# Kernel optimization log

Measured on AMD Instinct MI355X. Metric: run time of the kernel, lower is better.

Reference implementation:

```python
import jax, jax.numpy as jnp
import numpy as np

N = 2048       # nodes (also onehot length)
E = 32768      # edges (avg degree 16)
C_IN = 128
C_OUT = 128
OH_CH = 8
BN_EPS = 1e-5


def _conv1d(x, w):
    # x: [N, Cin, L], w: [Cout, Cin, 3], padding 1 (SAME)
    return jax.lax.conv_general_dilated(
        x, w, window_strides=(1,), padding=[(1, 1)],
        dimension_numbers=('NCH', 'OIH', 'NCH'))


def setup_inputs() -> dict:
    key = jax.random.key(0)
    ks = jax.random.split(key, 16)
    x = jax.random.normal(ks[0], (N, C_IN), dtype=jnp.float32)
    onehot = jax.random.uniform(ks[1], (N, N), dtype=jnp.float32)
    adj = jax.random.randint(ks[2], (2, E), 0, N)

    def lin(k, fan_in, shape):
        return jax.random.normal(k, shape, dtype=jnp.float32) / np.sqrt(fan_in)

    # first_linear: (C_IN + OH_CH) -> C_OUT  (stored as [in, out])
    W1 = lin(ks[3], C_IN + OH_CH, (C_IN + OH_CH, C_OUT))
    b1 = jnp.zeros((C_OUT,), jnp.float32)
    # mlp: BatchNorm1d(C_OUT) -> ReLU -> Linear(C_OUT, C_OUT)
    gamma = jnp.ones((C_OUT,), jnp.float32)
    beta = jnp.zeros((C_OUT,), jnp.float32)
    W2 = lin(ks[4], C_OUT, (C_OUT, C_OUT))
    b2 = jnp.zeros((C_OUT,), jnp.float32)
    # onehot_pipe: Conv1d(1,8,3) -> ReLU -> Conv1d(8,16,3) -> ReLU -> avgpool -> Linear(16, OH_CH)
    cw1 = lin(ks[5], 1 * 3, (8, 1, 3)); cb1 = jnp.zeros((8,), jnp.float32)
    cw2 = lin(ks[6], 8 * 3, (16, 8, 3)); cb2 = jnp.zeros((16,), jnp.float32)
    Wr = lin(ks[7], 16, (16, OH_CH)); br = jnp.zeros((OH_CH,), jnp.float32)

    return {"x": x, "onehot": onehot, "adj": adj, "n_nodes": N,
            "W1": W1, "b1": b1, "gamma": gamma, "beta": beta,
            "W2": W2, "b2": b2, "cw1": cw1, "cb1": cb1,
            "cw2": cw2, "cb2": cb2, "Wr": Wr, "br": br}


def reference(x, onehot, adj, n_nodes, W1, b1, gamma, beta, W2, b2,
              cw1, cb1, cw2, cb2, Wr, br):
    send, recv = adj[0], adj[1]
    # propagate: gather at senders, scatter-add at receivers
    agg_x = jax.ops.segment_sum(x[send], recv, num_segments=n_nodes)          # [N, C_IN]
    agg_oh = jax.ops.segment_sum(onehot[send], recv, num_segments=n_nodes)    # [N, N]
    new_oh = onehot + agg_oh                                                  # update()

    # onehot_pipe on sorted onehot rows
    s = jnp.sort(new_oh, axis=-1)[:, None, :]                                 # [N, 1, L]
    h = jax.nn.relu(_conv1d(s, cw1) + cb1[None, :, None])                     # [N, 8, L]
    h = jax.nn.relu(_conv1d(h, cw2) + cb2[None, :, None])                     # [N, 16, L]
    h = h.mean(axis=-1)                                                       # AdaptiveAvgPool1d(1)+Flatten
    readout = h @ Wr + br                                                     # [N, OH_CH]

    x2 = jnp.concatenate([agg_x, readout], axis=1)                            # hstack
    x2 = x2 @ W1 + b1                                                         # first_linear
    # BatchNorm1d in training mode (batch stats, biased variance)
    mu = x2.mean(axis=0)
    var = x2.var(axis=0)
    x2 = (x2 - mu) * jax.lax.rsqrt(var + BN_EPS) * gamma + beta
    x2 = jax.nn.relu(x2)
    x2 = x2 @ W2 + b2
    return (x2, new_oh)
```

## Files before the change

### kernel.cpp

```cpp
#include <hip/hip_runtime.h>
#include <hip/hip_bf16.h>
#include <math.h>

#define NN   2048
#define LROW 2048
#define DEGCAP 128

typedef __attribute__((ext_vector_type(8))) short short8;
typedef __attribute__((ext_vector_type(4))) float f32x4;
typedef unsigned int u32;

__device__ __forceinline__ unsigned short bf16b(float x) {
    __hip_bfloat16 h = __float2bfloat16(x);
    return *reinterpret_cast<unsigned short*>(&h);
}


__device__ __forceinline__ u32 pkmin(u32 a, u32 b) {
    u32 d; asm("v_pk_min_f16 %0, %1, %2" : "=v"(d) : "v"(a), "v"(b)); return d;
}
__device__ __forceinline__ u32 pkmax(u32 a, u32 b) {
    u32 d; asm("v_pk_max_f16 %0, %1, %2" : "=v"(d) : "v"(a), "v"(b)); return d;
}
__device__ __forceinline__ u32 packf2(float lo, float hi) {
    union { _Float16 h[2]; u32 u; } c;
    c.h[0] = (_Float16)lo; c.h[1] = (_Float16)hi;
    return c.u;
}
__device__ __forceinline__ float unpk_lo(u32 v) {
    union { u32 u; _Float16 h[2]; } c; c.u = v; return (float)c.h[0];
}
__device__ __forceinline__ float unpk_hi(u32 v) {
    union { u32 u; _Float16 h[2]; } c; c.u = v; return (float)c.h[1];
}


__global__ __launch_bounds__(256) void prep_k(
        const float* __restrict__ oh, unsigned short* __restrict__ ohbf,
        const int* __restrict__ send, const int* __restrict__ recv,
        int* __restrict__ cnt, int* __restrict__ elist2, int E) {
    const int bid = blockIdx.x;
    if (bid < NN) {
        int base = bid * 2048 + threadIdx.x * 8;
        float4 f0 = *(const float4*)(oh + base);
        float4 f1 = *(const float4*)(oh + base + 4);
        union { short8 s8; unsigned short us[8]; } pk;
        pk.us[0] = bf16b(f0.x); pk.us[1] = bf16b(f0.y);
        pk.us[2] = bf16b(f0.z); pk.us[3] = bf16b(f0.w);
        pk.us[4] = bf16b(f1.x); pk.us[5] = bf16b(f1.y);
        pk.us[6] = bf16b(f1.z); pk.us[7] = bf16b(f1.w);
        *(short8*)(ohbf + base) = pk.s8;
    } else {
        int i = (bid - NN) * 256 + threadIdx.x;
        if (i < E) {
            int r = recv[i];
            int slot = atomicAdd(&cnt[r], 1);
            if (slot < DEGCAP) elist2[r * DEGCAP + slot] = send[i];
        }
    }
}

__global__ void fill2_k(const int* __restrict__ send, const int* __restrict__ recv,
                        int* __restrict__ cnt, int* __restrict__ elist2, int E) {
    int i = blockIdx.x * blockDim.x + threadIdx.x;
    if (i >= E) return;
    int r = recv[i];
    int slot = atomicAdd(&cnt[r], 1);
    if (slot < DEGCAP) elist2[r * DEGCAP + slot] = send[i];
}


__device__ __forceinline__ void ce(float& a, float& b, bool up) {
    float lo = fminf(a, b), hi = fmaxf(a, b);
    a = up ? lo : hi;
    b = up ? hi : lo;
}

__device__ __forceinline__ void ce_pk(u32& a, u32& b, bool up) {
    u32 mn = pkmin(a, b), mx = pkmax(a, b);
    a = up ? mn : mx;
    b = up ? mx : mn;
}

__device__ __forceinline__ void merge8_pk(u32 h[4], bool up) {
    ce_pk(h[0], h[2], up); ce_pk(h[1], h[3], up);
    ce_pk(h[0], h[1], up); ce_pk(h[2], h[3], up);
#pragma unroll
    for (int m = 0; m < 4; ++m) {
        u32 hs = (h[m] >> 16) | (h[m] << 16);
        u32 mn = pkmin(h[m], hs);
        u32 mx = pkmax(h[m], hs);
        u32 ru = __builtin_amdgcn_perm(mx, mn, 0x07060100u);
        u32 rd = __builtin_amdgcn_perm(mn, mx, 0x07060100u);
        h[m] = up ? ru : rd;
    }
}

__device__ __forceinline__ short8 conv1pack(float xm, float x0v, float xp,
        const float* __restrict__ cw1, const float* __restrict__ cb1) {
    union { short8 s8; unsigned short us[8]; } pk;
#pragma unroll
    for (int c = 0; c < 8; ++c) {
        float w = cb1[c] + cw1[c * 3] * xm + cw1[c * 3 + 1] * x0v + cw1[c * 3 + 2] * xp;
        pk.us[c] = bf16b(w > 0.f ? w : 0.f);
    }
    return pk.s8;
}


template<int BF>
__global__ __launch_bounds__(256, 8) void fused_k(
        const float* __restrict__ oh, const unsigned short* __restrict__ ohbf,
        const float* __restrict__ x,
        const int* __restrict__ elist2, const int* __restrict__ cnt,
        float* __restrict__ newoh, float* __restrict__ t,
        const float* __restrict__ cw1, const float* __restrict__ cb1,
        const float* __restrict__ cw2, const float* __restrict__ cb2,
        const float* __restrict__ Wr,  const float* __restrict__ br,
        const float* __restrict__ W1,  const float* __restrict__ b1) {
    __shared__ __align__(16) char smem[1028 * 16];
    float* sf = (float*)smem;
    u32* sfu = (u32*)smem;
    unsigned short* h1t = (unsigned short*)smem;
    __shared__ unsigned short a_lds[16 * 32];
    __shared__ float red[4][16];
    __shared__ float u[136];
    __shared__ float lpart[128];

    const int r = blockIdx.x, tid = threadIdx.x;
    const int lane = tid & 63, wv = tid >> 6;
    const int col = tid * 8;

    for (int i = tid; i < 512; i += 256) {
        int c2 = i >> 5, k = i & 31, d = k >> 3, c1 = k & 7;
        float w = (d < 3) ? cw2[(c2 * 8 + c1) * 3 + d] : 0.f;
        a_lds[i] = bf16b(w);
    }

    float v[8];
    {
        float4 b0 = *(const float4*)(oh + (size_t)r * LROW + col);
        float4 b1v = *(const float4*)(oh + (size_t)r * LROW + col + 4);
        v[0] = b0.x;  v[1] = b0.y;  v[2] = b0.z;  v[3] = b0.w;
        v[4] = b1v.x; v[5] = b1v.y; v[6] = b1v.z; v[7] = b1v.w;
    }
    float myagg = 0.f;
    const int deg = min(cnt[r], DEGCAP);
    const int* my = elist2 + r * DEGCAP;
    int e = 0;
    if (BF) {
        for (; e + 4 <= deg; e += 4) {
            int se0 = my[e], se1 = my[e + 1], se2 = my[e + 2], se3 = my[e + 3];
            uint4 ua = *((const uint4*)(ohbf + (size_t)se0 * LROW) + tid);
            uint4 ub = *((const uint4*)(ohbf + (size_t)se1 * LROW) + tid);
            uint4 uc = *((const uint4*)(ohbf + (size_t)se2 * LROW) + tid);
            uint4 ud = *((const uint4*)(ohbf + (size_t)se3 * LROW) + tid);
            float xa = 0.f, xb = 0.f, xc = 0.f, xd = 0.f;
            if (tid < 128) {
                xa = x[(size_t)se0 * 128 + tid]; xb = x[(size_t)se1 * 128 + tid];
                xc = x[(size_t)se2 * 128 + tid]; xd = x[(size_t)se3 * 128 + tid];
            }
            v[0] += __uint_as_float(ua.x << 16); v[1] += __uint_as_float(ua.x & 0xffff0000u);
            v[2] += __uint_as_float(ua.y << 16); v[3] += __uint_as_float(ua.y & 0xffff0000u);
            v[4] += __uint_as_float(ua.z << 16); v[5] += __uint_as_float(ua.z & 0xffff0000u);
            v[6] += __uint_as_float(ua.w << 16); v[7] += __uint_as_float(ua.w & 0xffff0000u);
            v[0] += __uint_as_float(ub.x << 16); v[1] += __uint_as_float(ub.x & 0xffff0000u);
            v[2] += __uint_as_float(ub.y << 16); v[3] += __uint_as_float(ub.y & 0xffff0000u);
            v[4] += __uint_as_float(ub.z << 16); v[5] += __uint_as_float(ub.z & 0xffff0000u);
            v[6] += __uint_as_float(ub.w << 16); v[7] += __uint_as_float(ub.w & 0xffff0000u);
            v[0] += __uint_as_float(uc.x << 16); v[1] += __uint_as_float(uc.x & 0xffff0000u);
            v[2] += __uint_as_float(uc.y << 16); v[3] += __uint_as_float(uc.y & 0xffff0000u);
            v[4] += __uint_as_float(uc.z << 16); v[5] += __uint_as_float(uc.z & 0xffff0000u);
            v[6] += __uint_as_float(uc.w << 16); v[7] += __uint_as_float(uc.w & 0xffff0000u);
            v[0] += __uint_as_float(ud.x << 16); v[1] += __uint_as_float(ud.x & 0xffff0000u);
            v[2] += __uint_as_float(ud.y << 16); v[3] += __uint_as_float(ud.y & 0xffff0000u);
            v[4] += __uint_as_float(ud.z << 16); v[5] += __uint_as_float(ud.z & 0xffff0000u);
            v[6] += __uint_as_float(ud.w << 16); v[7] += __uint_as_float(ud.w & 0xffff0000u);
            myagg += xa; myagg += xb; myagg += xc; myagg += xd;
        }
        for (; e < deg; ++e) {
            int se = my[e];
            uint4 ua = *((const uint4*)(ohbf + (size_t)se * LROW) + tid);
            if (tid < 128) myagg += x[(size_t)se * 128 + tid];
            v[0] += __uint_as_float(ua.x << 16); v[1] += __uint_as_float(ua.x & 0xffff0000u);
            v[2] += __uint_as_float(ua.y << 16); v[3] += __uint_as_float(ua.y & 0xffff0000u);
            v[4] += __uint_as_float(ua.z << 16); v[5] += __uint_as_float(ua.z & 0xffff0000u);
            v[6] += __uint_as_float(ua.w << 16); v[7] += __uint_as_float(ua.w & 0xffff0000u);
        }
    } else {
        for (; e + 2 <= deg; e += 2) {
            int se0 = my[e], se1 = my[e + 1];
            float4 c0 = *(const float4*)(oh + (size_t)se0 * LROW + col);
            float4 c1 = *(const float4*)(oh + (size_t)se0 * LROW + col + 4);
            float4 d0 = *(const float4*)(oh + (size_t)se1 * LROW + col);
            float4 d1 = *(const float4*)(oh + (size_t)se1 * LROW + col + 4);
            float xa = 0.f, xb = 0.f;
            if (tid < 128) { xa = x[(size_t)se0 * 128 + tid]; xb = x[(size_t)se1 * 128 + tid]; }
            v[0] += c0.x; v[1] += c0.y; v[2] += c0.z; v[3] += c0.w;
            v[4] += c1.x; v[5] += c1.y; v[6] += c1.z; v[7] += c1.w;
            v[0] += d0.x; v[1] += d0.y; v[2] += d0.z; v[3] += d0.w;
            v[4] += d1.x; v[5] += d1.y; v[6] += d1.z; v[7] += d1.w;
            myagg += xa; myagg += xb;
        }
        for (; e < deg; ++e) {
            int se = my[e];
            float4 c0 = *(const float4*)(oh + (size_t)se * LROW + col);
            float4 c1 = *(const float4*)(oh + (size_t)se * LROW + col + 4);
            if (tid < 128) myagg += x[(size_t)se * 128 + tid];
            v[0] += c0.x; v[1] += c0.y; v[2] += c0.z; v[3] += c0.w;
            v[4] += c1.x; v[5] += c1.y; v[6] += c1.z; v[7] += c1.w;
        }
    }
    *(float4*)(newoh + (size_t)r * LROW + col)     = make_float4(v[0], v[1], v[2], v[3]);
    *(float4*)(newoh + (size_t)r * LROW + col + 4) = make_float4(v[4], v[5], v[6], v[7]);

    ce(v[0], v[1], true);  ce(v[2], v[3], false); ce(v[4], v[5], true);  ce(v[6], v[7], false);
    ce(v[0], v[2], true);  ce(v[1], v[3], true);  ce(v[4], v[6], false); ce(v[5], v[7], false);
    ce(v[0], v[1], true);  ce(v[2], v[3], true);  ce(v[4], v[5], false); ce(v[6], v[7], false);
    {
        bool up8 = (tid & 1) == 0;
        ce(v[0], v[4], up8); ce(v[1], v[5], up8); ce(v[2], v[6], up8); ce(v[3], v[7], up8);
        ce(v[0], v[2], up8); ce(v[1], v[3], up8); ce(v[4], v[6], up8); ce(v[5], v[7], up8);
        ce(v[0], v[1], up8); ce(v[2], v[3], up8); ce(v[4], v[5], up8); ce(v[6], v[7], up8);
    }

    u32 h[4];
    h[0] = packf2(v[0], v[1]);
    h[1] = packf2(v[2], v[3]);
    h[2] = packf2(v[4], v[5]);
    h[3] = packf2(v[6], v[7]);

#pragma unroll
    for (int lk = 4; lk <= 11; ++lk) {
        const int k = 1 << lk;
        const bool up = ((tid & (k >> 3)) == 0);
#pragma unroll
        for (int lj = lk - 1; lj >= 3; --lj) {
            const int D = 1 << (lj - 3);
            const bool keepmin = (((tid & D) == 0) == up);
            if (D <= 32) {
#pragma unroll
                for (int m = 0; m < 4; ++m) {
                    u32 hs = (u32)__shfl_xor((int)h[m], D, 64);
                    u32 mn = pkmin(h[m], hs), mx = pkmax(h[m], hs);
                    h[m] = keepmin ? mn : mx;
                }
            } else {
                __syncthreads();
                *(uint4*)&sfu[tid * 4] = make_uint4(h[0], h[1], h[2], h[3]);
                __syncthreads();
                uint4 P = *(const uint4*)&sfu[(tid ^ D) * 4];
                h[0] = keepmin ? pkmin(h[0], P.x) : pkmax(h[0], P.x);
                h[1] = keepmin ? pkmin(h[1], P.y) : pkmax(h[1], P.y);
                h[2] = keepmin ? pkmin(h[2], P.z) : pkmax(h[2], P.z);
                h[3] = keepmin ? pkmin(h[3], P.w) : pkmax(h[3], P.w);
            }
        }
        merge8_pk(h, up);
    }

    v[0] = unpk_lo(h[0]); v[1] = unpk_hi(h[0]);
    v[2] = unpk_lo(h[1]); v[3] = unpk_hi(h[1]);
    v[4] = unpk_lo(h[2]); v[5] = unpk_hi(h[2]);
    v[6] = unpk_lo(h[3]); v[7] = unpk_hi(h[3]);

    __syncthreads();
    *(float4*)&sf[col]     = make_float4(v[0], v[1], v[2], v[3]);
    *(float4*)&sf[col + 4] = make_float4(v[4], v[5], v[6], v[7]);
    __syncthreads();
    float lf1 = (tid == 0)   ? 0.f : sf[col - 1];
    float rt1 = (tid == 255) ? 0.f : sf[col + 8];

    short8 afrag = *(const short8*)&a_lds[(lane & 15) * 32 + (lane >> 4) * 8];
    const int mb = (lane >> 4) * 4;
    const float bs0 = cb2[mb], bs1 = cb2[mb + 1], bs2 = cb2[mb + 2], bs3 = cb2[mb + 3];
    float s0 = 0.f, s1 = 0.f, s2 = 0.f, s3 = 0.f;
    f32x4 zero = {0.f, 0.f, 0.f, 0.f};

#pragma unroll 1
    for (int half = 0; half < 2; ++half) {
        __syncthreads();
        if ((tid >> 7) == half) {
            const int lt = tid & 127;
#pragma unroll
            for (int p = 0; p < 8; ++p) {
                float xm  = (p == 0) ? lf1 : v[p - 1];
                float x0v = v[p];
                float xp  = (p == 7) ? rt1 : v[p + 1];
                int uu = lt * 8 + p + 1;
                int us = uu ^ ((uu >> 3) & 7);
                *(short8*)&h1t[us * 8] = conv1pack(xm, x0v, xp, cw1, cb1);
            }
        }
        if (half == 0) {
            if (tid == 128)
                *(short8*)&h1t[1025 * 8] = conv1pack(lf1, v[0], v[1], cw1, cb1);
            if (tid == 0) {
                short8 z = {0, 0, 0, 0, 0, 0, 0, 0};
                *(short8*)&h1t[0] = z;
            }
            if (tid == 1) {
                short8 z = {0, 0, 0, 0, 0, 0, 0, 0};
                *(short8*)&h1t[1026 * 8] = z;
                *(short8*)&h1t[1027 * 8] = z;
            }
        } else {
            if (tid == 127)
                *(short8*)&h1t[0] = conv1pack(v[6], v[7], rt1, cw1, cb1);
            if (tid == 0) {
                short8 z = {0, 0, 0, 0, 0, 0, 0, 0};
                *(short8*)&h1t[1025 * 8] = z;
            }
        }
        __syncthreads();

#pragma unroll 4
        for (int i = 0; i < 16; ++i) {
            int lp = (wv * 16 + i) * 16 + (lane & 15);
            int uu = lp + (lane >> 4);
            int us = uu ^ ((uu >> 3) & 7);
            short8 bfrag = *(const short8*)&h1t[us * 8];
            f32x4 d = __builtin_amdgcn_mfma_f32_16x16x32_bf16(afrag, bfrag, zero, 0, 0, 0);
            s0 += fmaxf(d[0] + bs0, 0.f);
            s1 += fmaxf(d[1] + bs1, 0.f);
            s2 += fmaxf(d[2] + bs2, 0.f);
            s3 += fmaxf(d[3] + bs3, 0.f);
        }
    }

#pragma unroll
    for (int off = 1; off < 16; off <<= 1) {
        s0 += __shfl_xor(s0, off);
        s1 += __shfl_xor(s1, off);
        s2 += __shfl_xor(s2, off);
        s3 += __shfl_xor(s3, off);
    }
    if ((lane & 15) == 0) {
        red[wv][mb + 0] = s0; red[wv][mb + 1] = s1;
        red[wv][mb + 2] = s2; red[wv][mb + 3] = s3;
    }
    if (tid < 128) u[tid] = myagg;
    __syncthreads();

    if (tid < 8) {
        float acc = br[tid];
#pragma unroll
        for (int c = 0; c < 16; ++c) {
            float tot = red[0][c] + red[1][c] + red[2][c] + red[3][c];
            acc += (tot * (1.0f / (float)LROW)) * Wr[c * 8 + tid];
        }
        u[128 + tid] = acc;
    }
    __syncthreads();

    {
        const int jc = tid & 127, hf = tid >> 7;
        float acc = (hf == 0) ? b1[jc] : 0.f;
        const int c0 = hf * 68;
#pragma unroll 4
        for (int c = 0; c < 68; ++c) acc += u[c0 + c] * W1[(size_t)(c0 + c) * 128 + jc];
        if (hf) lpart[jc] = acc;
        __syncthreads();
        if (!hf) t[(size_t)r * 128 + jc] = acc + lpart[jc];
    }
}


__global__ __launch_bounds__(256) void bnpart_k(const float* __restrict__ t,
                                                float* __restrict__ part) {
    const int b = blockIdx.x, tid = threadIdx.x;
    const int col = tid & 127, h = tid >> 7;
    float sm = 0.f, sq = 0.f;
    for (int i = 0; i < 32; ++i) {
        int row = b * 64 + h * 32 + i;
        float v = t[(size_t)row * 128 + col];
        sm += v; sq += v * v;
    }
    __shared__ float ps[2][128], pq[2][128];
    ps[h][col] = sm; pq[h][col] = sq;
    __syncthreads();
    if (h == 0) {
        part[(size_t)b * 256 + col]       = sm + ps[1][col];
        part[(size_t)b * 256 + 128 + col] = sq + pq[1][col];
    }
}


__global__ __launch_bounds__(256) void out_k(
        float* __restrict__ t, const float* __restrict__ part,
        const float* __restrict__ gamma, const float* __restrict__ beta,
        const float* __restrict__ W2, const float* __restrict__ b2) {
    __shared__ float u[16][128];
    __shared__ float sc_s[128], sh_s[128];
    const int r0 = blockIdx.x * 16, tid = threadIdx.x;
    if (tid < 128) {
        float sm = 0.f, sq = 0.f;
        for (int b = 0; b < 32; ++b) {
            sm += part[(size_t)b * 256 + tid];
            sq += part[(size_t)b * 256 + 128 + tid];
        }
        float mu  = sm / (float)NN;
        float var = sq / (float)NN - mu * mu;
        float sc  = rsqrtf(var + 1e-5f) * gamma[tid];
        sc_s[tid] = sc;
        sh_s[tid] = beta[tid] - mu * sc;
    }
    __syncthreads();
#pragma unroll
    for (int m = 0; m < 8; ++m) {
        int idx = tid + 256 * m;
        int rr = idx >> 7, c = idx & 127;
        float v = t[(size_t)(r0 + rr) * 128 + c];
        v = v * sc_s[c] + sh_s[c];
        u[rr][c] = v > 0.f ? v : 0.f;
    }
    __syncthreads();
    const int j = tid & 127, g = tid >> 7;
    float acc[8];
    float bb = b2[j];
#pragma unroll
    for (int rr = 0; rr < 8; ++rr) acc[rr] = bb;
    for (int c = 0; c < 128; ++c) {
        float w = W2[(size_t)c * 128 + j];
#pragma unroll
        for (int rr = 0; rr < 8; ++rr) acc[rr] += u[g * 8 + rr][c] * w;
    }
#pragma unroll
    for (int rr = 0; rr < 8; ++rr)
        t[(size_t)(r0 + g * 8 + rr) * 128 + j] = acc[rr];
}


extern "C" void kernel_launch(void* const* d_in, const int* in_sizes, int n_in,
                              void* d_out, int out_size, void* d_ws, size_t ws_size,
                              hipStream_t stream) {
    const float* x      = (const float*)d_in[0];
    const float* onehot = (const float*)d_in[1];
    const int*   adj    = (const int*)d_in[2];
    const float* W1     = (const float*)d_in[4];
    const float* b1     = (const float*)d_in[5];
    const float* gamma  = (const float*)d_in[6];
    const float* beta   = (const float*)d_in[7];
    const float* W2     = (const float*)d_in[8];
    const float* b2     = (const float*)d_in[9];
    const float* cw1    = (const float*)d_in[10];
    const float* cb1    = (const float*)d_in[11];
    const float* cw2    = (const float*)d_in[12];
    const float* cb2    = (const float*)d_in[13];
    const float* Wr     = (const float*)d_in[14];
    const float* br     = (const float*)d_in[15];

    const int E = in_sizes[2] / 2;
    const int* send = adj;
    const int* recv = adj + E;

    int*   cnt    = (int*)d_ws;
    int*   elist2 = cnt + 2048;
    float* part   = (float*)(elist2 + NN * DEGCAP);
    unsigned short* ohbf = (unsigned short*)(part + 32 * 256);
    size_t need = (size_t)((char*)(ohbf + (size_t)NN * LROW) - (char*)d_ws);
    const bool bf_path = (ws_size >= need);

    float* out_x2 = (float*)d_out;
    float* out_oh = out_x2 + (size_t)NN * 128;

    hipMemsetAsync(cnt, 0, 2048 * sizeof(int), stream);

    if (bf_path) {
        prep_k<<<NN + (E + 255) / 256, 256, 0, stream>>>(onehot, ohbf, send, recv,
                                                         cnt, elist2, E);
        fused_k<1><<<NN, 256, 0, stream>>>(onehot, ohbf, x, elist2, cnt,
                                           out_oh, out_x2,
                                           cw1, cb1, cw2, cb2, Wr, br, W1, b1);
    } else {
        fill2_k<<<(E + 255) / 256, 256, 0, stream>>>(send, recv, cnt, elist2, E);
        fused_k<0><<<NN, 256, 0, stream>>>(onehot, ohbf, x, elist2, cnt,
                                           out_oh, out_x2,
                                           cw1, cb1, cw2, cb2, Wr, br, W1, b1);
    }
    bnpart_k<<<32, 256, 0, stream>>>(out_x2, part);
    out_k<<<NN / 16, 256, 0, stream>>>(out_x2, part, gamma, beta, W2, b2);
}
```

Before: 80.62 us.

## Process two rows per block and interleave their bitonic sorts

The fused kernel now handles two onehot rows per block. It gathers and aggregates each row in turn, then runs both bitonic sorts together so every shuffle, LDS exchange and barrier serves two rows. The conv/readout tail is moved into a helper and called once per row. The grid is halved and launch bounds lowered, which cuts the number of resident blocks and the parallelism available to hide gather latency. The fallback path now reuses prep_k, which writes a bf16 copy even when the workspace check failed.

New measurement: 93.79 us. 16.3% more time.

```diff
diff --git a/kernel.cpp b/kernel.cpp
--- a/kernel.cpp
+++ b/kernel.cpp
@@ -60,15 +60,6 @@
     }
 }
 
-__global__ void fill2_k(const int* __restrict__ send, const int* __restrict__ recv,
-                        int* __restrict__ cnt, int* __restrict__ elist2, int E) {
-    int i = blockIdx.x * blockDim.x + threadIdx.x;
-    if (i >= E) return;
-    int r = recv[i];
-    int slot = atomicAdd(&cnt[r], 1);
-    if (slot < DEGCAP) elist2[r * DEGCAP + slot] = send[i];
-}
-
 
 __device__ __forceinline__ void ce(float& a, float& b, bool up) {
     float lo = fminf(a, b), hi = fmaxf(a, b);
@@ -108,8 +99,124 @@
 }
 
 
+__device__ __forceinline__ void conv_row(
+        const u32 h[4], float myagg, int r, int tid, int lane, int wv,
+        float* sf, unsigned short* h1t,
+        float (*red)[16], float* u, float* lpart,
+        short8 afrag, float bs0, float bs1, float bs2, float bs3,
+        const float* __restrict__ cw1, const float* __restrict__ cb1,
+        const float* __restrict__ Wr,  const float* __restrict__ br,
+        const float* __restrict__ W1,  const float* __restrict__ b1,
+        float* __restrict__ t) {
+    const int col = tid * 8;
+    float v[8];
+    v[0] = unpk_lo(h[0]); v[1] = unpk_hi(h[0]);
+    v[2] = unpk_lo(h[1]); v[3] = unpk_hi(h[1]);
+    v[4] = unpk_lo(h[2]); v[5] = unpk_hi(h[2]);
+    v[6] = unpk_lo(h[3]); v[7] = unpk_hi(h[3]);
+
+    __syncthreads();
+    *(float4*)&sf[col]     = make_float4(v[0], v[1], v[2], v[3]);
+    *(float4*)&sf[col + 4] = make_float4(v[4], v[5], v[6], v[7]);
+    __syncthreads();
+    float lf1 = (tid == 0)   ? 0.f : sf[col - 1];
+    float rt1 = (tid == 255) ? 0.f : sf[col + 8];
+
+    float s0 = 0.f, s1 = 0.f, s2 = 0.f, s3 = 0.f;
+    f32x4 zero = {0.f, 0.f, 0.f, 0.f};
+
+#pragma unroll 1
+    for (int half = 0; half < 2; ++half) {
+        __syncthreads();
+        if ((tid >> 7) == half) {
+            const int lt = tid & 127;
+#pragma unroll
+            for (int p = 0; p < 8; ++p) {
+                float xm  = (p == 0) ? lf1 : v[p - 1];
+                float x0v = v[p];
+                float xp  = (p == 7) ? rt1 : v[p + 1];
+                int uu = lt * 8 + p + 1;
+                int us = uu ^ ((uu >> 3) & 7);
+                *(short8*)&h1t[us * 8] = conv1pack(xm, x0v, xp, cw1, cb1);
+            }
+        }
+        if (half == 0) {
+            if (tid == 128)
+                *(short8*)&h1t[1025 * 8] = conv1pack(lf1, v[0], v[1], cw1, cb1);
+            if (tid == 0) {
+                short8 z = {0, 0, 0, 0, 0, 0, 0, 0};
+                *(short8*)&h1t[0] = z;
+            }
+            if (tid == 1) {
+                short8 z = {0, 0, 0, 0, 0, 0, 0, 0};
+                *(short8*)&h1t[1026 * 8] = z;
+                *(short8*)&h1t[1027 * 8] = z;
+            }
+        } else {
+            if (tid == 127)
+                *(short8*)&h1t[0] = conv1pack(v[6], v[7], rt1, cw1, cb1);
+            if (tid == 0) {
+                short8 z = {0, 0, 0, 0, 0, 0, 0, 0};
+                *(short8*)&h1t[1025 * 8] = z;
+            }
+        }
+        __syncthreads();
+
+#pragma unroll 4
+        for (int i = 0; i < 16; ++i) {
+            int lp = (wv * 16 + i) * 16 + (lane & 15);
+            int uu = lp + (lane >> 4);
+            int us = uu ^ ((uu >> 3) & 7);
+            short8 bfrag = *(const short8*)&h1t[us * 8];
+            f32x4 d = __builtin_amdgcn_mfma_f32_16x16x32_bf16(afrag, bfrag, zero, 0, 0, 0);
+            s0 += fmaxf(d[0] + bs0, 0.f);
+            s1 += fmaxf(d[1] + bs1, 0.f);
+            s2 += fmaxf(d[2] + bs2, 0.f);
+            s3 += fmaxf(d[3] + bs3, 0.f);
+        }
+    }
+
+#pragma unroll
+    for (int off = 1; off < 16; off <<= 1) {
+        s0 += __shfl_xor(s0, off);
+        s1 += __shfl_xor(s1, off);
+        s2 += __shfl_xor(s2, off);
+        s3 += __shfl_xor(s3, off);
+    }
+    const int mb = (lane >> 4) * 4;
+    if ((lane & 15) == 0) {
+        red[wv][mb + 0] = s0; red[wv][mb + 1] = s1;
+        red[wv][mb + 2] = s2; red[wv][mb + 3] = s3;
+    }
+    if (tid < 128) u[tid] = myagg;
+    __syncthreads();
+
+    if (tid < 8) {
+        float acc = br[tid];
+#pragma unroll
+        for (int c = 0; c < 16; ++c) {
+            float tot = red[0][c] + red[1][c] + red[2][c] + red[3][c];
+            acc += (tot * (1.0f / (float)LROW)) * Wr[c * 8 + tid];
+        }
+        u[128 + tid] = acc;
+    }
+    __syncthreads();
+
+    {
+        const int jc = tid & 127, hf = tid >> 7;
+        float acc = (hf == 0) ? b1[jc] : 0.f;
+        const int c0 = hf * 68;
+#pragma unroll 4
+        for (int c = 0; c < 68; ++c) acc += u[c0 + c] * W1[(size_t)(c0 + c) * 128 + jc];
+        if (hf) lpart[jc] = acc;
+        __syncthreads();
+        if (!hf) t[(size_t)r * 128 + jc] = acc + lpart[jc];
+    }
+}
+
+
 template<int BF>
-__global__ __launch_bounds__(256, 8) void fused_k(
+__global__ __launch_bounds__(256, 6) void fused2_k(
         const float* __restrict__ oh, const unsigned short* __restrict__ ohbf,
         const float* __restrict__ x,
         const int* __restrict__ elist2, const int* __restrict__ cnt,
@@ -127,9 +234,10 @@
     __shared__ float u[136];
     __shared__ float lpart[128];
 
-    const int r = blockIdx.x, tid = threadIdx.x;
+    const int tid = threadIdx.x;
     const int lane = tid & 63, wv = tid >> 6;
     const int col = tid * 8;
+    const int rA = blockIdx.x * 2, rB = rA + 1;
 
     for (int i = tid; i < 512; i += 256) {
         int c2 = i >> 5, k = i & 31, d = k >> 3, c1 = k & 7;
@@ -137,98 +245,94 @@
         a_lds[i] = bf16b(w);
     }
 
-    float v[8];
-    {
-        float4 b0 = *(const float4*)(oh + (size_t)r * LROW + col);
-        float4 b1v = *(const float4*)(oh + (size_t)r * LROW + col + 4);
-        v[0] = b0.x;  v[1] = b0.y;  v[2] = b0.z;  v[3] = b0.w;
-        v[4] = b1v.x; v[5] = b1v.y; v[6] = b1v.z; v[7] = b1v.w;
-    }
-    float myagg = 0.f;
-    const int deg = min(cnt[r], DEGCAP);
-    const int* my = elist2 + r * DEGCAP;
-    int e = 0;
-    if (BF) {
-        for (; e + 4 <= deg; e += 4) {
-            int se0 = my[e], se1 = my[e + 1], se2 = my[e + 2], se3 = my[e + 3];
-            uint4 ua = *((const uint4*)(ohbf + (size_t)se0 * LROW) + tid);
-            uint4 ub = *((const uint4*)(ohbf + (size_t)se1 * LROW) + tid);
-            uint4 uc = *((const uint4*)(ohbf + (size_t)se2 * LROW) + tid);
-            uint4 ud = *((const uint4*)(ohbf + (size_t)se3 * LROW) + tid);
-            float xa = 0.f, xb = 0.f, xc = 0.f, xd = 0.f;
-            if (tid < 128) {
-                xa = x[(size_t)se0 * 128 + tid]; xb = x[(size_t)se1 * 128 + tid];
-                xc = x[(size_t)se2 * 128 + tid]; xd = x[(size_t)se3 * 128 + tid];
-            }
-            v[0] += __uint_as_float(ua.x << 16); v[1] += __uint_as_float(ua.x & 0xffff0000u);
-            v[2] += __uint_as_float(ua.y << 16); v[3] += __uint_as_float(ua.y & 0xffff0000u);
-            v[4] += __uint_as_float(ua.z << 16); v[5] += __uint_as_float(ua.z & 0xffff0000u);
-            v[6] += __uint_as_float(ua.w << 16); v[7] += __uint_as_float(ua.w & 0xffff0000u);
-            v[0] += __uint_as_float(ub.x << 16); v[1] += __uint_as_float(ub.x & 0xffff0000u);
-            v[2] += __uint_as_float(ub.y << 16); v[3] += __uint_as_float(ub.y & 0xffff0000u);
-            v[4] += __uint_as_float(ub.z << 16); v[5] += __uint_as_float(ub.z & 0xffff0000u);
-            v[6] += __uint_as_float(ub.w << 16); v[7] += __uint_as_float(ub.w & 0xffff0000u);
-            v[0] += __uint_as_float(uc.x << 16); v[1] += __uint_as_float(uc.x & 0xffff0000u);
-            v[2] += __uint_as_float(uc.y << 16); v[3] += __uint_as_float(uc.y & 0xffff0000u);
-            v[4] += __uint_as_float(uc.z << 16); v[5] += __uint_as_float(uc.z & 0xffff0000u);
-            v[6] += __uint_as_float(uc.w << 16); v[7] += __uint_as_float(uc.w & 0xffff0000u);
-            v[0] += __uint_as_float(ud.x << 16); v[1] += __uint_as_float(ud.x & 0xffff0000u);
-            v[2] += __uint_as_float(ud.y << 16); v[3] += __uint_as_float(ud.y & 0xffff0000u);
-            v[4] += __uint_as_float(ud.z << 16); v[5] += __uint_as_float(ud.z & 0xffff0000u);
-            v[6] += __uint_as_float(ud.w << 16); v[7] += __uint_as_float(ud.w & 0xffff0000u);
-            myagg += xa; myagg += xb; myagg += xc; myagg += xd;
-        }
-        for (; e < deg; ++e) {
-            int se = my[e];
-            uint4 ua = *((const uint4*)(ohbf + (size_t)se * LROW) + tid);
-            if (tid < 128) myagg += x[(size_t)se * 128 + tid];
-            v[0] += __uint_as_float(ua.x << 16); v[1] += __uint_as_float(ua.x & 0xffff0000u);
-            v[2] += __uint_as_float(ua.y << 16); v[3] += __uint_as_float(ua.y & 0xffff0000u);
-            v[4] += __uint_as_float(ua.z << 16); v[5] += __uint_as_float(ua.z & 0xffff0000u);
-            v[6] += __uint_as_float(ua.w << 16); v[7] += __uint_as_float(ua.w & 0xffff0000u);
-        }
-    } else {
-        for (; e + 2 <= deg; e += 2) {
-            int se0 = my[e], se1 = my[e + 1];
-            float4 c0 = *(const float4*)(oh + (size_t)se0 * LROW + col);
-            float4 c1 = *(const float4*)(oh + (size_t)se0 * LROW + col + 4);
-            float4 d0 = *(const float4*)(oh + (size_t)se1 * LROW + col);
-            float4 d1 = *(const float4*)(oh + (size_t)se1 * LROW + col + 4);
-            float xa = 0.f, xb = 0.f;
-            if (tid < 128) { xa = x[(size_t)se0 * 128 + tid]; xb = x[(size_t)se1 * 128 + tid]; }
-            v[0] += c0.x; v[1] += c0.y; v[2] += c0.z; v[3] += c0.w;
-            v[4] += c1.x; v[5] += c1.y; v[6] += c1.z; v[7] += c1.w;
-            v[0] += d0.x; v[1] += d0.y; v[2] += d0.z; v[3] += d0.w;
-            v[4] += d1.x; v[5] += d1.y; v[6] += d1.z; v[7] += d1.w;
-            myagg += xa; myagg += xb;
-        }
-        for (; e < deg; ++e) {
-            int se = my[e];
-            float4 c0 = *(const float4*)(oh + (size_t)se * LROW + col);
-            float4 c1 = *(const float4*)(oh + (size_t)se * LROW + col + 4);
-            if (tid < 128) myagg += x[(size_t)se * 128 + tid];
-            v[0] += c0.x; v[1] += c0.y; v[2] += c0.z; v[3] += c0.w;
-            v[4] += c1.x; v[5] += c1.y; v[6] += c1.z; v[7] += c1.w;
-        }
-    }
-    *(float4*)(newoh + (size_t)r * LROW + col)     = make_float4(v[0], v[1], v[2], v[3]);
-    *(float4*)(newoh + (size_t)r * LROW + col + 4) = make_float4(v[4], v[5], v[6], v[7]);
-
-    ce(v[0], v[1], true);  ce(v[2], v[3], false); ce(v[4], v[5], true);  ce(v[6], v[7], false);
-    ce(v[0], v[2], true);  ce(v[1], v[3], true);  ce(v[4], v[6], false); ce(v[5], v[7], false);
-    ce(v[0], v[1], true);  ce(v[2], v[3], true);  ce(v[4], v[5], false); ce(v[6], v[7], false);
-    {
-        bool up8 = (tid & 1) == 0;
-        ce(v[0], v[4], up8); ce(v[1], v[5], up8); ce(v[2], v[6], up8); ce(v[3], v[7], up8);
-        ce(v[0], v[2], up8); ce(v[1], v[3], up8); ce(v[4], v[6], up8); ce(v[5], v[7], up8);
-        ce(v[0], v[1], up8); ce(v[2], v[3], up8); ce(v[4], v[5], up8); ce(v[6], v[7], up8);
-    }
-
-    u32 h[4];
-    h[0] = packf2(v[0], v[1]);
-    h[1] = packf2(v[2], v[3]);
-    h[2] = packf2(v[4], v[5]);
-    h[3] = packf2(v[6], v[7]);
+    u32 hA[4], hB[4];
+    float myaggA = 0.f, myaggB = 0.f;
+
+#pragma unroll 1
+    for (int row = 0; row < 2; ++row) {
+        const int r = row ? rB : rA;
+        float v[8];
+        {
+            float4 b0 = *(const float4*)(oh + (size_t)r * LROW + col);
+            float4 b1v = *(const float4*)(oh + (size_t)r * LROW + col + 4);
+            v[0] = b0.x;  v[1] = b0.y;  v[2] = b0.z;  v[3] = b0.w;
+            v[4] = b1v.x; v[5] = b1v.y; v[6] = b1v.z; v[7] = b1v.w;
+        }
+        float myagg = 0.f;
+        const int deg = min(cnt[r], DEGCAP);
+        const int* my = elist2 + r * DEGCAP;
+        int e = 0;
+        if (BF) {
+            for (; e + 4 <= deg; e += 4) {
+                int se0 = my[e], se1 = my[e + 1], se2 = my[e + 2], se3 = my[e + 3];
+                uint4 ua = *((const uint4*)(ohbf + (size_t)se0 * LROW) + tid);
+                uint4 ub = *((const uint4*)(ohbf + (size_t)se1 * LROW) + tid);
+                uint4 uc = *((const uint4*)(ohbf + (size_t)se2 * LROW) + tid);
+                uint4 ud = *((const uint4*)(ohbf + (size_t)se3 * LROW) + tid);
+                float xa = 0.f, xb = 0.f, xc = 0.f, xd = 0.f;
+                if (tid < 128) {
+                    xa = x[(size_t)se0 * 128 + tid]; xb = x[(size_t)se1 * 128 + tid];
+                    xc = x[(size_t)se2 * 128 + tid]; xd = x[(size_t)se3 * 128 + tid];
+                }
+                v[0] += __uint_as_float(ua.x << 16); v[1] += __uint_as_float(ua.x & 0xffff0000u);
+                v[2] += __uint_as_float(ua.y << 16); v[3] += __uint_as_float(ua.y & 0xffff0000u);
+                v[4] += __uint_as_float(ua.z << 16); v[5] += __uint_as_float(ua.z & 0xffff0000u);
+                v[6] += __uint_as_float(ua.w << 16); v[7] += __uint_as_float(ua.w & 0xffff0000u);
+                v[0] += __uint_as_float(ub.x << 16); v[1] += __uint_as_float(ub.x & 0xffff0000u);
+                v[2] += __uint_as_float(ub.y << 16); v[3] += __uint_as_float(ub.y & 0xffff0000u);
+                v[4] += __uint_as_float(ub.z << 16); v[5] += __uint_as_float(ub.z & 0xffff0000u);
+                v[6] += __uint_as_float(ub.w << 16); v[7] += __uint_as_float(ub.w & 0xffff0000u);
+                v[0] += __uint_as_float(uc.x << 16); v[1] += __uint_as_float(uc.x & 0xffff0000u);
+                v[2] += __uint_as_float(uc.y << 16); v[3] += __uint_as_float(uc.y & 0xffff0000u);
+                v[4] += __uint_as_float(uc.z << 16); v[5] += __uint_as_float(uc.z & 0xffff0000u);
+                v[6] += __uint_as_float(uc.w << 16); v[7] += __uint_as_float(uc.w & 0xffff0000u);
+                v[0] += __uint_as_float(ud.x << 16); v[1] += __uint_as_float(ud.x & 0xffff0000u);
+                v[2] += __uint_as_float(ud.y << 16); v[3] += __uint_as_float(ud.y & 0xffff0000u);
+                v[4] += __uint_as_float(ud.z << 16); v[5] += __uint_as_float(ud.z & 0xffff0000u);
+                v[6] += __uint_as_float(ud.w << 16); v[7] += __uint_as_float(ud.w & 0xffff0000u);
+                myagg += xa; myagg += xb; myagg += xc; myagg += xd;
+            }
+            for (; e < deg; ++e) {
+                int se = my[e];
+                uint4 ua = *((const uint4*)(ohbf + (size_t)se * LROW) + tid);
+                if (tid < 128) myagg += x[(size_t)se * 128 + tid];
+                v[0] += __uint_as_float(ua.x << 16); v[1] += __uint_as_float(ua.x & 0xffff0000u);
+                v[2] += __uint_as_float(ua.y << 16); v[3] += __uint_as_float(ua.y & 0xffff0000u);
+                v[4] += __uint_as_float(ua.z << 16); v[5] += __uint_as_float(ua.z & 0xffff0000u);
+                v[6] += __uint_as_float(ua.w << 16); v[7] += __uint_as_float(ua.w & 0xffff0000u);
+            }
+        } else {
+            for (; e < deg; ++e) {
+                int se = my[e];
+                float4 c0 = *(const float4*)(oh + (size_t)se * LROW + col);
+                float4 c1 = *(const float4*)(oh + (size_t)se * LROW + col + 4);
+                if (tid < 128) myagg += x[(size_t)se * 128 + tid];
+                v[0] += c0.x; v[1] += c0.y; v[2] += c0.z; v[3] += c0.w;
+                v[4] += c1.x; v[5] += c1.y; v[6] += c1.z; v[7] += c1.w;
+            }
+        }
+        *(float4*)(newoh + (size_t)r * LROW + col)     = make_float4(v[0], v[1], v[2], v[3]);
+        *(float4*)(newoh + (size_t)r * LROW + col + 4) = make_float4(v[4], v[5], v[6], v[7]);
+
+        ce(v[0], v[1], true);  ce(v[2], v[3], false); ce(v[4], v[5], true);  ce(v[6], v[7], false);
+        ce(v[0], v[2], true);  ce(v[1], v[3], true);  ce(v[4], v[6], false); ce(v[5], v[7], false);
+        ce(v[0], v[1], true);  ce(v[2], v[3], true);  ce(v[4], v[5], false); ce(v[6], v[7], false);
+        {
+            bool up8 = (tid & 1) == 0;
+            ce(v[0], v[4], up8); ce(v[1], v[5], up8); ce(v[2], v[6], up8); ce(v[3], v[7], up8);
+            ce(v[0], v[2], up8); ce(v[1], v[3], up8); ce(v[4], v[6], up8); ce(v[5], v[7], up8);
+            ce(v[0], v[1], up8); ce(v[2], v[3], up8); ce(v[4], v[5], up8); ce(v[6], v[7], up8);
+        }
+        if (row == 0) {
+            hA[0] = packf2(v[0], v[1]); hA[1] = packf2(v[2], v[3]);
+            hA[2] = packf2(v[4], v[5]); hA[3] = packf2(v[6], v[7]);
+            myaggA = myagg;
+        } else {
+            hB[0] = packf2(v[0], v[1]); hB[1] = packf2(v[2], v[3]);
+            hB[2] = packf2(v[4], v[5]); hB[3] = packf2(v[6], v[7]);
+            myaggB = myagg;
+        }
+    }
 
 #pragma unroll
     for (int lk = 4; lk <= 11; ++lk) {
@@ -241,128 +345,40 @@
             if (D <= 32) {
 #pragma unroll
                 for (int m = 0; m < 4; ++m) {
-                    u32 hs = (u32)__shfl_xor((int)h[m], D, 64);
-                    u32 mn = pkmin(h[m], hs), mx = pkmax(h[m], hs);
-                    h[m] = keepmin ? mn : mx;
+                    u32 hsA = (u32)__shfl_xor((int)hA[m], D, 64);
+                    u32 hsB = (u32)__shfl_xor((int)hB[m], D, 64);
+                    hA[m] = keepmin ? pkmin(hA[m], hsA) : pkmax(hA[m], hsA);
+                    hB[m] = keepmin ? pkmin(hB[m], hsB) : pkmax(hB[m], hsB);
                 }
             } else {
                 __syncthreads();
-                *(uint4*)&sfu[tid * 4] = make_uint4(h[0], h[1], h[2], h[3]);
+                *(uint4*)&sfu[tid * 4]        = make_uint4(hA[0], hA[1], hA[2], hA[3]);
+                *(uint4*)&sfu[1024 + tid * 4] = make_uint4(hB[0], hB[1], hB[2], hB[3]);
                 __syncthreads();
-                uint4 P = *(const uint4*)&sfu[(tid ^ D) * 4];
-                h[0] = keepmin ? pkmin(h[0], P.x) : pkmax(h[0], P.x);
-                h[1] = keepmin ? pkmin(h[1], P.y) : pkmax(h[1], P.y);
-                h[2] = keepmin ? pkmin(h[2], P.z) : pkmax(h[2], P.z);
-                h[3] = keepmin ? pkmin(h[3], P.w) : pkmax(h[3], P.w);
-            }
-        }
-        merge8_pk(h, up);
-    }
-
-    v[0] = unpk_lo(h[0]); v[1] = unpk_hi(h[0]);
-    v[2] = unpk_lo(h[1]); v[3] = unpk_hi(h[1]);
-    v[4] = unpk_lo(h[2]); v[5] = unpk_hi(h[2]);
-    v[6] = unpk_lo(h[3]); v[7] = unpk_hi(h[3]);
-
-    __syncthreads();
-    *(float4*)&sf[col]     = make_float4(v[0], v[1], v[2], v[3]);
-    *(float4*)&sf[col + 4] = make_float4(v[4], v[5], v[6], v[7]);
-    __syncthreads();
-    float lf1 = (tid == 0)   ? 0.f : sf[col - 1];
-    float rt1 = (tid == 255) ? 0.f : sf[col + 8];
+                uint4 PA = *(const uint4*)&sfu[(tid ^ D) * 4];
+                uint4 PB = *(const uint4*)&sfu[1024 + (tid ^ D) * 4];
+                hA[0] = keepmin ? pkmin(hA[0], PA.x) : pkmax(hA[0], PA.x);
+                hA[1] = keepmin ? pkmin(hA[1], PA.y) : pkmax(hA[1], PA.y);
+                hA[2] = keepmin ? pkmin(hA[2], PA.z) : pkmax(hA[2], PA.z);
+                hA[3] = keepmin ? pkmin(hA[3], PA.w) : pkmax(hA[3], PA.w);
+                hB[0] = keepmin ? pkmin(hB[0], PB.x) : pkmax(hB[0], PB.x);
+                hB[1] = keepmin ? pkmin(hB[1], PB.y) : pkmax(hB[1], PB.y);
+                hB[2] = keepmin ? pkmin(hB[2], PB.z) : pkmax(hB[2], PB.z);
+                hB[3] = keepmin ? pkmin(hB[3], PB.w) : pkmax(hB[3], PB.w);
+            }
+        }
+        merge8_pk(hA, up);
+        merge8_pk(hB, up);
+    }
 
     short8 afrag = *(const short8*)&a_lds[(lane & 15) * 32 + (lane >> 4) * 8];
     const int mb = (lane >> 4) * 4;
     const float bs0 = cb2[mb], bs1 = cb2[mb + 1], bs2 = cb2[mb + 2], bs3 = cb2[mb + 3];
-    float s0 = 0.f, s1 = 0.f, s2 = 0.f, s3 = 0.f;
-    f32x4 zero = {0.f, 0.f, 0.f, 0.f};
-
-#pragma unroll 1
-    for (int half = 0; half < 2; ++half) {
-        __syncthreads();
-        if ((tid >> 7) == half) {
-            const int lt = tid & 127;
-#pragma unroll
-            for (int p = 0; p < 8; ++p) {
-                float xm  = (p == 0) ? lf1 : v[p - 1];
-                float x0v = v[p];
-                float xp  = (p == 7) ? rt1 : v[p + 1];
-                int uu = lt * 8 + p + 1;
-                int us = uu ^ ((uu >> 3) & 7);
-                *(short8*)&h1t[us * 8] = conv1pack(xm, x0v, xp, cw1, cb1);
-            }
-        }
-        if (half == 0) {
-            if (tid == 128)
-                *(short8*)&h1t[1025 * 8] = conv1pack(lf1, v[0], v[1], cw1, cb1);
-            if (tid == 0) {
-                short8 z = {0, 0, 0, 0, 0, 0, 0, 0};
-                *(short8*)&h1t[0] = z;
-            }
-            if (tid == 1) {
-                short8 z = {0, 0, 0, 0, 0, 0, 0, 0};
-                *(short8*)&h1t[1026 * 8] = z;
-                *(short8*)&h1t[1027 * 8] = z;
-            }
-        } else {
-            if (tid == 127)
-                *(short8*)&h1t[0] = conv1pack(v[6], v[7], rt1, cw1, cb1);
-            if (tid == 0) {
-                short8 z = {0, 0, 0, 0, 0, 0, 0, 0};
-                *(short8*)&h1t[1025 * 8] = z;
-            }
-        }
-        __syncthreads();
-
-#pragma unroll 4
-        for (int i = 0; i < 16; ++i) {
-            int lp = (wv * 16 + i) * 16 + (lane & 15);
-            int uu = lp + (lane >> 4);
-            int us = uu ^ ((uu >> 3) & 7);
-            short8 bfrag = *(const short8*)&h1t[us * 8];
-            f32x4 d = __builtin_amdgcn_mfma_f32_16x16x32_bf16(afrag, bfrag, zero, 0, 0, 0);
-            s0 += fmaxf(d[0] + bs0, 0.f);
-            s1 += fmaxf(d[1] + bs1, 0.f);
-            s2 += fmaxf(d[2] + bs2, 0.f);
-            s3 += fmaxf(d[3] + bs3, 0.f);
-        }
-    }
-
-#pragma unroll
-    for (int off = 1; off < 16; off <<= 1) {
-        s0 += __shfl_xor(s0, off);
-        s1 += __shfl_xor(s1, off);
-        s2 += __shfl_xor(s2, off);
-        s3 += __shfl_xor(s3, off);
-    }
-    if ((lane & 15) == 0) {
-        red[wv][mb + 0] = s0; red[wv][mb + 1] = s1;
-        red[wv][mb + 2] = s2; red[wv][mb + 3] = s3;
-    }
-    if (tid < 128) u[tid] = myagg;
-    __syncthreads();
-
-    if (tid < 8) {
-        float acc = br[tid];
-#pragma unroll
-        for (int c = 0; c < 16; ++c) {
-            float tot = red[0][c] + red[1][c] + red[2][c] + red[3][c];
-            acc += (tot * (1.0f / (float)LROW)) * Wr[c * 8 + tid];
-        }
-        u[128 + tid] = acc;
-    }
-    __syncthreads();
-
-    {
-        const int jc = tid & 127, hf = tid >> 7;
-        float acc = (hf == 0) ? b1[jc] : 0.f;
-        const int c0 = hf * 68;
-#pragma unroll 4
-        for (int c = 0; c < 68; ++c) acc += u[c0 + c] * W1[(size_t)(c0 + c) * 128 + jc];
-        if (hf) lpart[jc] = acc;
-        __syncthreads();
-        if (!hf) t[(size_t)r * 128 + jc] = acc + lpart[jc];
-    }
+
+    conv_row(hA, myaggA, rA, tid, lane, wv, sf, h1t, red, u, lpart,
+             afrag, bs0, bs1, bs2, bs3, cw1, cb1, Wr, br, W1, b1, t);
+    conv_row(hB, myaggB, rB, tid, lane, wv, sf, h1t, red, u, lpart,
+             afrag, bs0, bs1, bs2, bs3, cw1, cb1, Wr, br, W1, b1, t);
 }
 
 
@@ -469,14 +485,15 @@
     if (bf_path) {
         prep_k<<<NN + (E + 255) / 256, 256, 0, stream>>>(onehot, ohbf, send, recv,
                                                          cnt, elist2, E);
-        fused_k<1><<<NN, 256, 0, stream>>>(onehot, ohbf, x, elist2, cnt,
-                                           out_oh, out_x2,
-                                           cw1, cb1, cw2, cb2, Wr, br, W1, b1);
+        fused2_k<1><<<NN / 2, 256, 0, stream>>>(onehot, ohbf, x, elist2, cnt,
+                                                out_oh, out_x2,
+                                                cw1, cb1, cw2, cb2, Wr, br, W1, b1);
     } else {
-        fill2_k<<<(E + 255) / 256, 256, 0, stream>>>(send, recv, cnt, elist2, E);
-        fused_k<0><<<NN, 256, 0, stream>>>(onehot, ohbf, x, elist2, cnt,
-                                           out_oh, out_x2,
-                                           cw1, cb1, cw2, cb2, Wr, br, W1, b1);
+        prep_k<<<NN + (E + 255) / 256, 256, 0, stream>>>(onehot, ohbf, send, recv,
+                                                         cnt, elist2, E);
+        fused2_k<0><<<NN / 2, 256, 0, stream>>>(onehot, ohbf, x, elist2, cnt,
+                                                out_oh, out_x2,
+                                                cw1, cb1, cw2, cb2, Wr, br, W1, b1);
     }
     bnpart_k<<<32, 256, 0, stream>>>(out_x2, part);
     out_k<<<NN / 16, 256, 0, stream>>>(out_x2, part, gamma, beta, W2, b2);
```
